# Optimization experiments

Measured on AMD Instinct MI355X. Metric: run time of the kernel, lower is better.

Reference implementation:

```python
import jax, jax.numpy as jnp
from jax import lax
import numpy as np

INPUT_SIZE = 3
RESERVOIR = 2048
OUTPUT_SIZE = 3
SPECTRAL_RADIUS = 0.9
SPARSITY = 0.1
B, T = 16, 2048


def setup_inputs() -> dict:
    key = jax.random.key(0)
    kx, kwin, kw, kmask, kwo, kb = jax.random.split(key, 6)
    x = jax.random.normal(kx, (B, T, INPUT_SIZE), dtype=jnp.float32)
    Win = jax.random.normal(kwin, (RESERVOIR, INPUT_SIZE), dtype=jnp.float32)
    W = jax.random.normal(kw, (RESERVOIR, RESERVOIR), dtype=jnp.float32)
    # spectral-radius rescale (circular law: rho(randn(R,R)) ~ sqrt(R)), then sparsify
    W = W * (SPECTRAL_RADIUS / jnp.sqrt(jnp.float32(RESERVOIR)))
    mask = (jax.random.uniform(kmask, (RESERVOIR, RESERVOIR)) < SPARSITY).astype(jnp.float32)
    W = W * mask
    bound = 1.0 / np.sqrt(RESERVOIR)
    Wout_w = jax.random.uniform(kwo, (OUTPUT_SIZE, RESERVOIR), minval=-bound, maxval=bound, dtype=jnp.float32)
    Wout_b = jax.random.uniform(kb, (OUTPUT_SIZE,), minval=-bound, maxval=bound, dtype=jnp.float32)
    return {"x": x, "Win": Win, "W": W, "Wout_w": Wout_w, "Wout_b": Wout_b}


def reference(x, Win, W, Wout_w, Wout_b):
    Bsz = x.shape[0]
    R = W.shape[0]
    h0 = jnp.zeros((Bsz, R), dtype=x.dtype)

    def step(h, xt):
        h_new = jnp.tanh(xt @ Win.T + h @ W.T)  # [B, R]
        return h_new, h_new

    _, hs = lax.scan(step, h0, jnp.swapaxes(x, 0, 1))  # hs: [T, B, R]
    outs = hs @ Wout_w.T + Wout_b  # [T, B, O]
    return jnp.swapaxes(outs, 0, 1)  # [B, T, O]
```

## Files before the change

kernel.cpp:

```cpp
#include <hip/hip_runtime.h>
#include <math.h>


#define RDIM   2048
#define BATCH  16
#define TSTEPS 2048
#define NIN    3
#define NOUT   3
#define NBLK   256
#define NTHR   512

typedef unsigned u32x2 __attribute__((ext_vector_type(2)));

#define HT0_DW     0
#define HT1_DW     16384
#define WS_USED_DW 32768

#define POLL_MAX   (1L << 14)

#define TAGOK(a, b, t) (((a)[0] >> 16) == (t) && ((a)[1] >> 16) == (t) && \
                        ((b)[0] >> 16) == (t) && ((b)[1] >> 16) == (t))

__device__ __forceinline__ void st1_uc(unsigned* p, unsigned v) {
    asm volatile("global_store_dword %0, %1, off sc0 sc1" :: "v"(p), "v"(v) : "memory");
}
__device__ __forceinline__ void pf_issue(u32x2& a, u32x2& b,
                                         const unsigned* pA, const unsigned* pB) {
    asm volatile("global_load_dwordx2 %0, %2, off sc0 sc1\n\t"
                 "global_load_dwordx2 %1, %3, off sc0 sc1"
                 : "+v"(a), "+v"(b) : "v"(pA), "v"(pB) : "memory");
}

__device__ __forceinline__ int q8(float v) {
    float c = fminf(127.f, fmaxf(-127.f, v));
    return (int)__builtin_rintf(c);
}
__device__ __forceinline__ float fast_tanh(float x) {
    float e2 = __expf(2.f * x);
    return 1.f - 2.f * __builtin_amdgcn_rcpf(e2 + 1.f);
}
__device__ __forceinline__ unsigned pack4(int a, int b, int c, int d) {
    return (a & 0xff) | ((b & 0xff) << 8) | ((c & 0xff) << 16) | ((d & 0xff) << 24);
}
__device__ __forceinline__ int dot4i(unsigned a, unsigned b, int c) {
#if __has_builtin(__builtin_amdgcn_sdot4)
    return __builtin_amdgcn_sdot4((int)a, (int)b, c, false);
#else
    c += (int)(signed char)(a) * (int)(signed char)(b);
    c += (int)(signed char)(a >> 8)  * (int)(signed char)(b >> 8);
    c += (int)(signed char)(a >> 16) * (int)(signed char)(b >> 16);
    c += (int)(signed char)(a >> 24) * (int)(signed char)(b >> 24);
    return c;
#endif
}
__device__ __forceinline__ int dot16(uint4 wq, uint4 hq, int c) {
    c = dot4i(wq.x, hq.x, c);
    c = dot4i(wq.y, hq.y, c);
    c = dot4i(wq.z, hq.z, c);
    c = dot4i(wq.w, hq.w, c);
    return c;
}

extern "C" __global__ void __launch_bounds__(NTHR, 1) esn_persist(
    const float* __restrict__ W,
    const float* __restrict__ Win,
    const float* __restrict__ x,
    const float* __restrict__ Wout,
    const float* __restrict__ bout,
    unsigned* wsu,
    float* __restrict__ out)
{
    __shared__ int red[2][8][8][17];
    __shared__ __align__(16) unsigned hstage[2][2][512];
    __shared__ float wscale[64];
    extern __shared__ unsigned wlds[];

    const int tid  = threadIdx.x;
    const int lane = tid & 63;
    const int w    = tid >> 6;
    const int blk  = blockIdx.x;
    const int rg   = blk & 31;
    const int g    = blk >> 5;
    const int b0    = g * 2;
    const int kslot = lane >> 3;
    const int rgrp  = lane & 7;

#pragma unroll
    for (int rr = 0; rr < 8; ++rr) {
        const int   row = rg * 64 + w * 8 + rr;
        const float4* Wr = (const float4*)(W + (size_t)row * RDIM);
        float m = 0.f;
#pragma unroll
        for (int j = 0; j < 8; ++j) {
            float4 v = Wr[j * 64 + lane];
            m = fmaxf(m, fmaxf(fmaxf(fabsf(v.x), fabsf(v.y)),
                               fmaxf(fabsf(v.z), fabsf(v.w))));
        }
#pragma unroll
        for (int off = 32; off >= 1; off >>= 1)
            m = fmaxf(m, __shfl_xor(m, off, 64));
        const float inv = (m > 0.f) ? 127.f / m : 0.f;
        if (lane == 0) wscale[w * 8 + rr] = (m > 0.f) ? m / 127.f : 0.f;
#pragma unroll
        for (int j = 0; j < 8; ++j) {
            float4 v = Wr[j * 64 + lane];
            const int gsw = (j * 16 + (lane >> 2)) ^ w;
            wlds[(w * 8 + rr) * 512 + gsw * 4 + (lane & 3)] =
                pack4(q8(v.x * inv), q8(v.y * inv), q8(v.z * inv), q8(v.w * inv));
        }
    }

    float wn0 = 0.f, wn1 = 0.f, wn2 = 0.f;
    if (tid < 128) {
        const float* wp = Win + (size_t)(rg * 64 + (tid >> 1)) * NIN;
        wn0 = wp[0]; wn1 = wp[1]; wn2 = wp[2];
    }
    __syncthreads();

    unsigned* const ht0 = wsu + HT0_DW;
    unsigned* const ht1 = wsu + HT1_DW;

    u32x2 ta = {0, 0}, tb = {0, 0}, tae = {0, 0}, tbe = {0, 0};
    {
        const unsigned* pA0 = ht0 + g * 2048 +        128 * w + 2 * lane;
        const unsigned* pB0 = ht0 + g * 2048 + 1024 + 128 * w + 2 * lane;
        pf_issue(tae, tbe, pA0, pB0);
        pf_issue(ta,  tb,  pA0, pB0);
    }
    int dly = 6;

    for (int t = 0; t <= TSTEPS; ++t) {
        unsigned* const hb  = (t & 1) ? ht1 : ht0;
        unsigned* const hbn = (t & 1) ? ht0 : ht1;
        const unsigned tg  = (unsigned)t & 0xffffu;
        const unsigned tg1 = (unsigned)(t + 1) & 0xffffu;
        const int par = t & 1;

        bool first_hit;
        {
            const unsigned* pA = hb + g * 2048 +        128 * w + 2 * lane;
            const unsigned* pB = hb + g * 2048 + 1024 + 128 * w + 2 * lane;
            if (w < 2 && t > 0)
                asm volatile("s_waitcnt vmcnt(3)" : "+v"(tae), "+v"(tbe) :: "memory");
            else
                asm volatile("s_waitcnt vmcnt(2)" : "+v"(tae), "+v"(tbe) :: "memory");
            bool ok = TAGOK(tae, tbe, tg);
            if (ok) { ta = tae; tb = tbe; }
            if (!ok) {
                asm volatile("s_waitcnt vmcnt(0)" : "+v"(ta), "+v"(tb) :: "memory");
                ok = TAGOK(ta, tb, tg);
            }
            first_hit = ok;
            long r = 0;
            while (!ok && r <= POLL_MAX) {
                ++r;
                if (r > 1) __builtin_amdgcn_s_sleep(2);
                asm volatile("global_load_dwordx2 %0, %2, off sc0 sc1\n\t"
                             "global_load_dwordx2 %1, %3, off sc0 sc1\n\t"
                             "s_waitcnt vmcnt(0)"
                             : "+v"(ta), "+v"(tb) : "v"(pA), "v"(pB) : "memory");
                ok = TAGOK(ta, tb, tg);
            }
        }
        dly += __all((int)first_hit) ? -1 : 4;
        dly = dly < 0 ? 0 : (dly > 24 ? 24 : dly);

        const unsigned pdA = (ta[0] & 0xffffu) | (ta[1] << 16);
        const unsigned pdB = (tb[0] & 0xffffu) | (tb[1] << 16);
        hstage[par][0][(w << 6) + lane] = pdA;
        hstage[par][1][(w << 6) + lane] = pdB;

        float xv0 = 0.f, xv1 = 0.f, xv2 = 0.f;
        if (t < TSTEPS && tid < 128) {
            const float* xp = x + ((size_t)(b0 + (tid & 1)) * TSTEPS + t) * NIN;
            xv0 = xp[0]; xv1 = xp[1]; xv2 = xp[2];
        }

        if (t < TSTEPS) {
            const uint4* hwA = (const uint4*)&hstage[par][0][(w << 6) + (kslot << 3)];
            const uint4* hwB = (const uint4*)&hstage[par][1][(w << 6) + (kslot << 3)];
            const uint4 hA0 = hwA[0], hA1 = hwA[1];
            const uint4 hB0 = hwB[0], hB1 = hwB[1];

            int acc[8][2];
#pragma unroll
            for (int rr = 0; rr < 8; ++rr) { acc[rr][0] = 0; acc[rr][1] = 0; }
            const uint4* w4p = (const uint4*)wlds;
            const int g0 = (w << 4) + (((kslot << 1) ^ rgrp) & 15);
#pragma unroll
            for (int rr = 0; rr < 8; ++rr) {
                const int gi = (((rgrp << 3) + rr) << 7);
                uint4 w0 = w4p[gi + g0];
                uint4 w1 = w4p[gi + (g0 ^ 1)];
                acc[rr][0] = dot16(w0, hA0, acc[rr][0]);
                acc[rr][0] = dot16(w1, hA1, acc[rr][0]);
                acc[rr][1] = dot16(w0, hB0, acc[rr][1]);
                acc[rr][1] = dot16(w1, hB1, acc[rr][1]);
            }
#pragma unroll
            for (int rr = 0; rr < 8; ++rr)
#pragma unroll
                for (int b = 0; b < 2; ++b) {
                    int a = acc[rr][b];
                    a += __shfl_xor(a, 8, 64);
                    a += __shfl_xor(a, 16, 64);
                    a += __shfl_xor(a, 32, 64);
                    acc[rr][b] = a;
                }
            if (lane < 8) {
#pragma unroll
                for (int rr = 0; rr < 8; ++rr) {
                    red[par][w][lane][(rr << 1)]     = acc[rr][0];
                    red[par][w][lane][(rr << 1) + 1] = acc[rr][1];
                }
            }
        }
        __syncthreads();

        if (t < TSTEPS) {
            asm volatile("s_waitcnt vmcnt(0)"
                         : "+v"(ta), "+v"(tb), "+v"(tae), "+v"(tbe) :: "memory");
            const unsigned* nA = hbn + g * 2048 +        128 * w + 2 * lane;
            const unsigned* nB = hbn + g * 2048 + 1024 + 128 * w + 2 * lane;
            pf_issue(tae, tbe, nA, nB);
        }

        if (t < TSTEPS && tid < 128) {
            const int br = tid >> 1;
            const int b  = tid & 1;
            int s = 0;
#pragma unroll
            for (int wp = 0; wp < 8; ++wp)
                s += red[par][wp][br >> 3][((br & 7) << 1) + b];
            float pre = (float)s * wscale[br] * (1.f / 127.f)
                      + wn0 * xv0 + wn1 * xv1 + wn2 * xv2;
            const int qv = q8(fast_tanh(pre) * 127.f);
            const int qlo = __shfl(qv, ((lane >> 1) << 2) + (lane & 1), 64);
            const int qhi = __shfl(qv, ((lane >> 1) << 2) + 2 + (lane & 1), 64);
            if (lane < 32) {
                const int bb = lane & 1;
                const int u  = (w << 4) + (lane >> 1);
                unsigned dv = (unsigned)(qlo & 0xff) |
                              ((unsigned)(qhi & 0xff) << 8) | (tg1 << 16);
                st1_uc(hbn + g * 2048 + bb * 1024 + rg * 32 + u, dv);
            }
        }

        if (t < TSTEPS) {
            for (int i = 0; i < dly; ++i) __builtin_amdgcn_s_sleep(1);
            const unsigned* nA = hbn + g * 2048 +        128 * w + 2 * lane;
            const unsigned* nB = hbn + g * 2048 + 1024 + 128 * w + 2 * lane;
            pf_issue(ta, tb, nA, nB);
        }

        if (t > 0 && rg == ((t - 1) & 31) && w >= 2) {
            const int pw = w - 2;
            const int b  = pw / NOUT;
            const int k  = pw % NOUT;
            const float4* wo4 = (const float4*)(Wout + (size_t)k * RDIM);
            float a = 0.f;
#pragma unroll
            for (int j = 0; j < 8; ++j) {
                unsigned hv = hstage[par][b][(lane << 3) + j];
                float4 wf = wo4[(lane << 3) + j];
                a += (float)(int)(signed char)(hv & 0xff)         * wf.x;
                a += (float)(int)(signed char)((hv >> 8) & 0xff)  * wf.y;
                a += (float)(int)(signed char)((hv >> 16) & 0xff) * wf.z;
                a += (float)(int)(signed char)(hv >> 24)          * wf.w;
            }
#pragma unroll
            for (int off = 32; off >= 1; off >>= 1)
                a += __shfl_xor(a, off, 64);
            if (lane == 0)
                out[((size_t)(b0 + b) * TSTEPS + (t - 1)) * NOUT + k] =
                    a * (1.f / 127.f) + bout[k];
        }
    }
}

extern "C" void kernel_launch(void* const* d_in, const int* in_sizes, int n_in,
                              void* d_out, int out_size, void* d_ws, size_t ws_size,
                              hipStream_t stream) {
    const float* x    = (const float*)d_in[0];
    const float* Win  = (const float*)d_in[1];
    const float* W    = (const float*)d_in[2];
    const float* Wout = (const float*)d_in[3];
    const float* bout = (const float*)d_in[4];
    float* out = (float*)d_out;
    unsigned* wsu = (unsigned*)d_ws;

    hipMemsetAsync(d_ws, 0, (size_t)WS_USED_DW * sizeof(unsigned), stream);

    hipFuncSetAttribute((const void*)esn_persist,
                        hipFuncAttributeMaxDynamicSharedMemorySize, 131072);

    void* args[] = {(void*)&W, (void*)&Win, (void*)&x, (void*)&Wout, (void*)&bout,
                    (void*)&wsu, (void*)&out};
    hipError_t e = hipLaunchCooperativeKernel((const void*)esn_persist,
                                              dim3(NBLK), dim3(NTHR),
                                              args, 131072, stream);
    if (e != hipSuccess) {
        esn_persist<<<dim3(NBLK), dim3(NTHR), 131072, stream>>>(
            W, Win, x, Wout, bout, wsu, out);
    }
}
```

Baseline: 6.481 ms.

## Remap blocks onto XCDs so each batch group exchanges state within one L2

At startup each block reads its hardware XCC id and takes a slot through an atomic counter, so all 32 blocks of a batch group land on the same XCD. A probe then checks that stores with sc0 only are visible to the other blocks through the shared L2. If every block confirms, the per-step hidden-state exchange uses sc0-only loads and stores (L2 scope) in place of sc0 sc1 system-coherent accesses; otherwise it falls back to the old mapping. The early-prefetch double buffer (tae/tbe) is removed, which risks exposing more polling latency, and relying on L2 visibility across CUs is fragile.

```diff
diff --git a/kernel.cpp b/kernel.cpp
--- a/kernel.cpp
+++ b/kernel.cpp
@@ -14,21 +14,64 @@
 
 #define HT0_DW     0
 #define HT1_DW     16384
-#define WS_USED_DW 32768
+#define DISC_DW    32768
+#define RPT_DW     32776
+#define PPT_DW     33032
+#define PRB_DW     33288
+#define DEC_DW     33544
+#define WS_USED_DW 33552
 
 #define POLL_MAX   (1L << 14)
 
 #define TAGOK(a, b, t) (((a)[0] >> 16) == (t) && ((a)[1] >> 16) == (t) && \
                         ((b)[0] >> 16) == (t) && ((b)[1] >> 16) == (t))
 
-__device__ __forceinline__ void st1_uc(unsigned* p, unsigned v) {
-    asm volatile("global_store_dword %0, %1, off sc0 sc1" :: "v"(p), "v"(v) : "memory");
-}
-__device__ __forceinline__ void pf_issue(u32x2& a, u32x2& b,
-                                         const unsigned* pA, const unsigned* pB) {
-    asm volatile("global_load_dwordx2 %0, %2, off sc0 sc1\n\t"
-                 "global_load_dwordx2 %1, %3, off sc0 sc1"
-                 : "+v"(a), "+v"(b) : "v"(pA), "v"(pB) : "memory");
+__device__ __forceinline__ unsigned sysld(const unsigned* p) {
+    return __hip_atomic_load(p, __ATOMIC_RELAXED, __HIP_MEMORY_SCOPE_SYSTEM);
+}
+__device__ __forceinline__ void sysst(unsigned* p, unsigned v) {
+    __hip_atomic_store(p, v, __ATOMIC_RELAXED, __HIP_MEMORY_SCOPE_SYSTEM);
+}
+__device__ __forceinline__ void st1_l2(unsigned* p, unsigned v) {
+    asm volatile("global_store_dword %0, %1, off sc0" :: "v"(p), "v"(v) : "memory");
+}
+__device__ __forceinline__ unsigned ld1_l2(const unsigned* p) {
+    unsigned d;
+    asm volatile("global_load_dword %0, %1, off sc0\n\ts_waitcnt vmcnt(0)"
+                 : "=v"(d) : "v"(p) : "memory");
+    return d;
+}
+__device__ __forceinline__ void pf_issue_p(u32x2& a, u32x2& b,
+                                           const unsigned* pA, const unsigned* pB,
+                                           bool fast) {
+    if (fast)
+        asm volatile("global_load_dwordx2 %0, %2, off sc0\n\t"
+                     "global_load_dwordx2 %1, %3, off sc0"
+                     : "+v"(a), "+v"(b) : "v"(pA), "v"(pB) : "memory");
+    else
+        asm volatile("global_load_dwordx2 %0, %2, off sc0 sc1\n\t"
+                     "global_load_dwordx2 %1, %3, off sc0 sc1"
+                     : "+v"(a), "+v"(b) : "v"(pA), "v"(pB) : "memory");
+}
+__device__ __forceinline__ void ld_poll_p(u32x2& a, u32x2& b,
+                                          const unsigned* pA, const unsigned* pB,
+                                          bool fast) {
+    if (fast)
+        asm volatile("global_load_dwordx2 %0, %2, off sc0\n\t"
+                     "global_load_dwordx2 %1, %3, off sc0\n\t"
+                     "s_waitcnt vmcnt(0)"
+                     : "+v"(a), "+v"(b) : "v"(pA), "v"(pB) : "memory");
+    else
+        asm volatile("global_load_dwordx2 %0, %2, off sc0 sc1\n\t"
+                     "global_load_dwordx2 %1, %3, off sc0 sc1\n\t"
+                     "s_waitcnt vmcnt(0)"
+                     : "+v"(a), "+v"(b) : "v"(pA), "v"(pB) : "memory");
+}
+__device__ __forceinline__ void st1_p(unsigned* p, unsigned v, bool fast) {
+    if (fast)
+        asm volatile("global_store_dword %0, %1, off sc0" :: "v"(p), "v"(v) : "memory");
+    else
+        asm volatile("global_store_dword %0, %1, off sc0 sc1" :: "v"(p), "v"(v) : "memory");
 }
 
 __device__ __forceinline__ int q8(float v) {
@@ -73,17 +116,67 @@
     __shared__ int red[2][8][8][17];
     __shared__ __align__(16) unsigned hstage[2][2][512];
     __shared__ float wscale[64];
+    __shared__ int s_map[3];
     extern __shared__ unsigned wlds[];
 
     const int tid  = threadIdx.x;
     const int lane = tid & 63;
     const int w    = tid >> 6;
     const int blk  = blockIdx.x;
-    const int rg   = blk & 31;
-    const int g    = blk >> 5;
-    const int b0    = g * 2;
     const int kslot = lane >> 3;
     const int rgrp  = lane & 7;
+
+    if (tid == 0) {
+        unsigned xcc;
+        asm volatile("s_getreg_b32 %0, hwreg(20, 0, 32)" : "=s"(xcc));
+        xcc &= 7u;
+        unsigned slot = atomicAdd(&wsu[DISC_DW + xcc], 1u);
+        __builtin_amdgcn_s_waitcnt(0);
+        sysst(&wsu[RPT_DW + blk], (slot < 32u) ? 1u : 2u);
+        s_map[0] = (int)xcc;
+        s_map[1] = (int)(slot & 31u);
+    }
+    __syncthreads();
+    const int gx = s_map[0], rgx = s_map[1];
+
+    if (tid == 0) st1_l2(&wsu[PRB_DW + gx * 32 + rgx], 0xC0DEu);
+    if (w == 0) {
+        bool got = false;
+        for (long r = 0; r < (1L << 13) && !got; ++r) {
+            unsigned v = 0xC0DEu;
+            if (lane < 32) v = ld1_l2(&wsu[PRB_DW + gx * 32 + lane]);
+            got = (bool)__all((int)(v == 0xC0DEu));
+            if (!got) __builtin_amdgcn_s_sleep(2);
+        }
+        if (lane == 0) sysst(&wsu[PPT_DW + blk], got ? 1u : 2u);
+    }
+    if (blk == 0) {
+        bool ok = true;
+        if (tid < NBLK) {
+            unsigned m = 0, p = 0;
+            for (long r = 0; r < (1L << 20) && (m == 0 || p == 0); ++r) {
+                m = sysld(&wsu[RPT_DW + tid]);
+                p = sysld(&wsu[PPT_DW + tid]);
+                if (m == 0 || p == 0) __builtin_amdgcn_s_sleep(2);
+            }
+            ok = (m == 1u && p == 1u);
+        }
+        ok = (bool)__syncthreads_and((int)ok);
+        if (tid == 0) sysst(&wsu[DEC_DW], ok ? 2u : 1u);
+    }
+    if (tid == 0) {
+        unsigned d = 0;
+        for (long r = 0; r < (1L << 20) && d == 0; ++r) {
+            d = sysld(&wsu[DEC_DW]);
+            if (d == 0) __builtin_amdgcn_s_sleep(2);
+        }
+        s_map[2] = (d == 2u) ? 1 : 0;
+    }
+    __syncthreads();
+    const bool fastp = s_map[2] != 0;
+    const int g  = fastp ? gx  : (blk >> 5);
+    const int rg = fastp ? rgx : (blk & 31);
+    const int b0 = g * 2;
 
 #pragma unroll
     for (int rr = 0; rr < 8; ++rr) {
@@ -120,12 +213,11 @@
     unsigned* const ht0 = wsu + HT0_DW;
     unsigned* const ht1 = wsu + HT1_DW;
 
-    u32x2 ta = {0, 0}, tb = {0, 0}, tae = {0, 0}, tbe = {0, 0};
+    u32x2 ta = {0, 0}, tb = {0, 0};
     {
         const unsigned* pA0 = ht0 + g * 2048 +        128 * w + 2 * lane;
         const unsigned* pB0 = ht0 + g * 2048 + 1024 + 128 * w + 2 * lane;
-        pf_issue(tae, tbe, pA0, pB0);
-        pf_issue(ta,  tb,  pA0, pB0);
+        pf_issue_p(ta, tb, pA0, pB0, fastp);
     }
     int dly = 6;
 
@@ -140,25 +232,14 @@
         {
             const unsigned* pA = hb + g * 2048 +        128 * w + 2 * lane;
             const unsigned* pB = hb + g * 2048 + 1024 + 128 * w + 2 * lane;
-            if (w < 2 && t > 0)
-                asm volatile("s_waitcnt vmcnt(3)" : "+v"(tae), "+v"(tbe) :: "memory");
-            else
-                asm volatile("s_waitcnt vmcnt(2)" : "+v"(tae), "+v"(tbe) :: "memory");
-            bool ok = TAGOK(tae, tbe, tg);
-            if (ok) { ta = tae; tb = tbe; }
-            if (!ok) {
-                asm volatile("s_waitcnt vmcnt(0)" : "+v"(ta), "+v"(tb) :: "memory");
-                ok = TAGOK(ta, tb, tg);
-            }
+            asm volatile("s_waitcnt vmcnt(0)" : "+v"(ta), "+v"(tb) :: "memory");
+            bool ok = TAGOK(ta, tb, tg);
             first_hit = ok;
             long r = 0;
             while (!ok && r <= POLL_MAX) {
                 ++r;
                 if (r > 1) __builtin_amdgcn_s_sleep(2);
-                asm volatile("global_load_dwordx2 %0, %2, off sc0 sc1\n\t"
-                             "global_load_dwordx2 %1, %3, off sc0 sc1\n\t"
-                             "s_waitcnt vmcnt(0)"
-                             : "+v"(ta), "+v"(tb) : "v"(pA), "v"(pB) : "memory");
+                ld_poll_p(ta, tb, pA, pB, fastp);
                 ok = TAGOK(ta, tb, tg);
             }
         }
@@ -216,14 +297,6 @@
             }
         }
         __syncthreads();
-
-        if (t < TSTEPS) {
-            asm volatile("s_waitcnt vmcnt(0)"
-                         : "+v"(ta), "+v"(tb), "+v"(tae), "+v"(tbe) :: "memory");
-            const unsigned* nA = hbn + g * 2048 +        128 * w + 2 * lane;
-            const unsigned* nB = hbn + g * 2048 + 1024 + 128 * w + 2 * lane;
-            pf_issue(tae, tbe, nA, nB);
-        }
 
         if (t < TSTEPS && tid < 128) {
             const int br = tid >> 1;
@@ -242,7 +315,7 @@
                 const int u  = (w << 4) + (lane >> 1);
                 unsigned dv = (unsigned)(qlo & 0xff) |
                               ((unsigned)(qhi & 0xff) << 8) | (tg1 << 16);
-                st1_uc(hbn + g * 2048 + bb * 1024 + rg * 32 + u, dv);
+                st1_p(hbn + g * 2048 + bb * 1024 + rg * 32 + u, dv, fastp);
             }
         }
 
@@ -250,7 +323,7 @@
             for (int i = 0; i < dly; ++i) __builtin_amdgcn_s_sleep(1);
             const unsigned* nA = hbn + g * 2048 +        128 * w + 2 * lane;
             const unsigned* nB = hbn + g * 2048 + 1024 + 128 * w + 2 * lane;
-            pf_issue(ta, tb, nA, nB);
+            pf_issue_p(ta, tb, nA, nB, fastp);
         }
 
         if (t > 0 && rg == ((t - 1) & 31) && w >= 2) {
```

Measured after the change: 7.930 ms. 1.22x slower.
